# Kernel optimization log

Measured on AMD Instinct MI355X. Metric: run time of the kernel, lower is better.

## Reference

```python
import jax, jax.numpy as jnp
import numpy as np

LOSS_WEIGHT = 1.0

def setup_inputs() -> dict:
    key = jax.random.key(0)
    k1, k2 = jax.random.split(key)
    point_set_1 = jax.random.normal(k1, (8, 4096, 2), dtype=jnp.float32)
    point_set_2 = jax.random.normal(k2, (8, 4096, 2), dtype=jnp.float32)
    return {"point_set_1": point_set_1, "point_set_2": point_set_2}

def reference(point_set_1, point_set_2):
    # Pairwise L2 distances: C[n, i, j] = ||x[n,i] - y[n,j]||_2  -> (N, P1, P2)
    diff = point_set_1[:, :, None, :] - point_set_2[:, None, :, :]
    C = jnp.sqrt(jnp.sum(diff * diff, axis=-1))
    d1 = jnp.min(C, axis=-1).mean(axis=-1)  # x -> nearest y
    d2 = jnp.min(C, axis=-2).mean(axis=-1)  # y -> nearest x
    dist = (d1 + d2) / 2.0                   # (N,)
    return dist * LOSS_WEIGHT
```

## Files before the change

### kernel.cpp

```cpp
#include <hip/hip_runtime.h>
#include <hip/hip_bf16.h>
#include <math.h>


#define B 8
#define N 4096
#define BLOCK 256
#define TX 8
#define NI 2
#define NT 16

__global__ __launch_bounds__(BLOCK) void chamfer_stage1(
    const float2* __restrict__ P1, const float2* __restrict__ P2,
    float* __restrict__ partial, int nj, int jc) {
  extern __shared__ float4 yb[];

  int b = blockIdx.x;
  int c = b % nj; b /= nj;
  int itile = b % NI; b /= NI;
  int n = b % B;
  int dir = b / B;

  const float2* __restrict__ Q = dir ? P2 : P1;
  const float2* __restrict__ D = dir ? P1 : P2;

  const float2* dbase = D + n * N + c * jc;
  for (int t = threadIdx.x; t < jc; t += BLOCK) {
    float2 p = dbase[t];
    yb[t] = make_float4(-2.0f * p.x, -2.0f * p.y,
                        fmaf(p.x, p.x, p.y * p.y), 0.0f);
  }
  __syncthreads();

  float qx[TX], qy[TX], m[TX];
  const float2* qbase = Q + n * N + itile * (BLOCK * TX) + threadIdx.x;
#pragma unroll
  for (int k = 0; k < TX; ++k) {
    float2 q = qbase[k * BLOCK];
    qx[k] = q.x; qy[k] = q.y;
    m[k] = INFINITY;
  }

#pragma unroll 4
  for (int j = 0; j < jc; ++j) {
    float4 y = yb[j];
#pragma unroll
    for (int k = 0; k < TX; ++k) {
      float t = fmaf(qx[k], y.x, fmaf(qy[k], y.y, y.z));
      m[k] = fminf(m[k], t);
    }
  }

  float* dst = partial + (((size_t)c * 2 + dir) * B + n) * N
             + itile * (BLOCK * TX) + threadIdx.x;
#pragma unroll
  for (int k = 0; k < TX; ++k) dst[k * BLOCK] = m[k];
}

__global__ __launch_bounds__(BLOCK) void chamfer_stage2(
    const float2* __restrict__ P1, const float2* __restrict__ P2,
    const float* __restrict__ partial, float* __restrict__ bs, int nj) {
  int b = blockIdx.x;
  int t = b % NT; b /= NT;
  int n = b % B;
  int dir = b / B;

  const float2* __restrict__ Q = dir ? P2 : P1;
  int i = t * BLOCK + threadIdx.x;

  float m = INFINITY;
  const float* __restrict__ pbase = partial + ((size_t)dir * B + n) * N + i;
#pragma unroll 4
  for (int c = 0; c < nj; ++c)
    m = fminf(m, pbase[(size_t)c * 2 * B * N]);

  float2 q = Q[n * N + i];
  float d2 = m + fmaf(q.x, q.x, q.y * q.y);
  float sum = sqrtf(fmaxf(d2, 0.0f));

  __shared__ float red[BLOCK];
  red[threadIdx.x] = sum;
  __syncthreads();
  for (int s = BLOCK / 2; s > 0; s >>= 1) {
    if (threadIdx.x < s) red[threadIdx.x] += red[threadIdx.x + s];
    __syncthreads();
  }
  if (threadIdx.x == 0) bs[(dir * B + n) * NT + t] = red[0];
}

__global__ __launch_bounds__(64) void chamfer_stage3(
    const float* __restrict__ bs, float* __restrict__ out) {
  int n = blockIdx.x;
  int lane = threadIdx.x;
  float v = 0.0f;
  if (lane < 2 * NT) {
    int dir = lane / NT, t = lane % NT;
    v = bs[(dir * B + n) * NT + t];
  }
#pragma unroll
  for (int s = 32; s > 0; s >>= 1)
    v += __shfl_down(v, s, 64);
  if (lane == 0) out[n] = v * (0.5f / (float)N);
}

extern "C" void kernel_launch(void* const* d_in, const int* in_sizes, int n_in,
                              void* d_out, int out_size, void* d_ws, size_t ws_size,
                              hipStream_t stream) {
  const float2* P1 = (const float2*)d_in[0];
  const float2* P2 = (const float2*)d_in[1];
  float* out = (float*)d_out;
  float* partial = (float*)d_ws;

  size_t bs_bytes = 2 * B * NT * sizeof(float);
  int nj = 16;
  while (nj > 1 && (size_t)nj * 2 * B * N * sizeof(float) + bs_bytes > ws_size) nj >>= 1;
  int jc = N / nj;

  float* bs = partial + (size_t)nj * 2 * B * N;

  chamfer_stage1<<<dim3(2 * B * NI * nj), BLOCK, jc * sizeof(float4), stream>>>(
      P1, P2, partial, nj, jc);
  chamfer_stage2<<<dim3(2 * B * NT), BLOCK, 0, stream>>>(P1, P2, partial, bs, nj);
  chamfer_stage3<<<dim3(B), 64, 0, stream>>>(bs, out);
}
```

Before: 30.05 us.

## Use packed FP32 FMA with min3, drop LDS staging, retile to 32 queries per thread

Stage 1 now runs 128-thread blocks, each thread holding 32 query points as packed float2 pairs and computing two candidate points per step with inline v_pk_fma_f32 and v_min3_f32. The LDS staging of transformed candidates is removed, and candidates are read straight from global memory with their -2x and norm terms recomputed in-loop. The j-split grows to 64 chunks, which makes the partial buffer larger and stage 2's reduction longer. The workspace-size check is also removed, so the code assumes the workspace can hold 64 chunks.

```diff
diff --git a/kernel.cpp b/kernel.cpp
--- a/kernel.cpp
+++ b/kernel.cpp
@@ -3,85 +3,95 @@
 #include <math.h>
 
 
+typedef float f32x2 __attribute__((ext_vector_type(2)));
+
 #define B 8
 #define N 4096
-#define BLOCK 256
-#define TX 8
-#define NI 2
+#define NJ 64
+#define JC (N / NJ)
+#define S1B 128
+#define TX 32
 #define NT 16
+#define S2B 256
 
-__global__ __launch_bounds__(BLOCK) void chamfer_stage1(
+__global__ __launch_bounds__(S1B, 2) void chamfer_stage1(
     const float2* __restrict__ P1, const float2* __restrict__ P2,
-    float* __restrict__ partial, int nj, int jc) {
-  extern __shared__ float4 yb[];
-
+    float* __restrict__ partial) {
   int b = blockIdx.x;
-  int c = b % nj; b /= nj;
-  int itile = b % NI; b /= NI;
+  int c = b % NJ; b /= NJ;
   int n = b % B;
   int dir = b / B;
 
   const float2* __restrict__ Q = dir ? P2 : P1;
   const float2* __restrict__ D = dir ? P1 : P2;
+  const float2* __restrict__ db = D + n * N + c * JC;
 
-  const float2* dbase = D + n * N + c * jc;
-  for (int t = threadIdx.x; t < jc; t += BLOCK) {
-    float2 p = dbase[t];
-    yb[t] = make_float4(-2.0f * p.x, -2.0f * p.y,
-                        fmaf(p.x, p.x, p.y * p.y), 0.0f);
-  }
-  __syncthreads();
-
-  float qx[TX], qy[TX], m[TX];
-  const float2* qbase = Q + n * N + itile * (BLOCK * TX) + threadIdx.x;
+  f32x2 qx[TX / 2], qy[TX / 2];
+  float m[TX];
+  const float2* qbase = Q + n * N + threadIdx.x;
 #pragma unroll
-  for (int k = 0; k < TX; ++k) {
-    float2 q = qbase[k * BLOCK];
-    qx[k] = q.x; qy[k] = q.y;
-    m[k] = INFINITY;
+  for (int p = 0; p < TX / 2; ++p) {
+    float2 q0 = qbase[(2 * p) * S1B];
+    float2 q1 = qbase[(2 * p + 1) * S1B];
+    qx[p] = (f32x2){q0.x, q1.x};
+    qy[p] = (f32x2){q0.y, q1.y};
+    m[2 * p] = INFINITY;
+    m[2 * p + 1] = INFINITY;
   }
 
 #pragma unroll 4
-  for (int j = 0; j < jc; ++j) {
-    float4 y = yb[j];
+  for (int j = 0; j < JC; j += 2) {
+    float2 p0 = db[j];
+    float2 p1 = db[j + 1];
+    float ax0f = -2.f * p0.x, ay0f = -2.f * p0.y;
+    float s0f = fmaf(p0.x, p0.x, p0.y * p0.y);
+    float ax1f = -2.f * p1.x, ay1f = -2.f * p1.y;
+    float s1f = fmaf(p1.x, p1.x, p1.y * p1.y);
+    f32x2 ax0 = {ax0f, ax0f}, ay0 = {ay0f, ay0f}, ss0 = {s0f, s0f};
+    f32x2 ax1 = {ax1f, ax1f}, ay1 = {ay1f, ay1f}, ss1 = {s1f, s1f};
 #pragma unroll
-    for (int k = 0; k < TX; ++k) {
-      float t = fmaf(qx[k], y.x, fmaf(qy[k], y.y, y.z));
-      m[k] = fminf(m[k], t);
+    for (int p = 0; p < TX / 2; ++p) {
+      f32x2 u0, t0, u1, t1;
+      asm("v_pk_fma_f32 %0, %1, %2, %3" : "=v"(u0) : "v"(qy[p]), "v"(ay0), "v"(ss0));
+      asm("v_pk_fma_f32 %0, %1, %2, %3" : "=v"(t0) : "v"(qx[p]), "v"(ax0), "v"(u0));
+      asm("v_pk_fma_f32 %0, %1, %2, %3" : "=v"(u1) : "v"(qy[p]), "v"(ay1), "v"(ss1));
+      asm("v_pk_fma_f32 %0, %1, %2, %3" : "=v"(t1) : "v"(qx[p]), "v"(ax1), "v"(u1));
+      asm("v_min3_f32 %0, %0, %1, %2" : "+v"(m[2 * p])     : "v"(t0.x), "v"(t1.x));
+      asm("v_min3_f32 %0, %0, %1, %2" : "+v"(m[2 * p + 1]) : "v"(t0.y), "v"(t1.y));
     }
   }
 
-  float* dst = partial + (((size_t)c * 2 + dir) * B + n) * N
-             + itile * (BLOCK * TX) + threadIdx.x;
+  float* __restrict__ dst =
+      partial + (((size_t)c * 2 + dir) * B + n) * N + threadIdx.x;
 #pragma unroll
-  for (int k = 0; k < TX; ++k) dst[k * BLOCK] = m[k];
+  for (int k = 0; k < TX; ++k) dst[k * S1B] = m[k];
 }
 
-__global__ __launch_bounds__(BLOCK) void chamfer_stage2(
+__global__ __launch_bounds__(S2B) void chamfer_stage2(
     const float2* __restrict__ P1, const float2* __restrict__ P2,
-    const float* __restrict__ partial, float* __restrict__ bs, int nj) {
+    const float* __restrict__ partial, float* __restrict__ bs) {
   int b = blockIdx.x;
   int t = b % NT; b /= NT;
   int n = b % B;
   int dir = b / B;
 
   const float2* __restrict__ Q = dir ? P2 : P1;
-  int i = t * BLOCK + threadIdx.x;
+  int i = t * S2B + threadIdx.x;
 
   float m = INFINITY;
   const float* __restrict__ pbase = partial + ((size_t)dir * B + n) * N + i;
-#pragma unroll 4
-  for (int c = 0; c < nj; ++c)
+#pragma unroll 8
+  for (int c = 0; c < NJ; ++c)
     m = fminf(m, pbase[(size_t)c * 2 * B * N]);
 
   float2 q = Q[n * N + i];
   float d2 = m + fmaf(q.x, q.x, q.y * q.y);
   float sum = sqrtf(fmaxf(d2, 0.0f));
 
-  __shared__ float red[BLOCK];
+  __shared__ float red[S2B];
   red[threadIdx.x] = sum;
   __syncthreads();
-  for (int s = BLOCK / 2; s > 0; s >>= 1) {
+  for (int s = S2B / 2; s > 0; s >>= 1) {
     if (threadIdx.x < s) red[threadIdx.x] += red[threadIdx.x + s];
     __syncthreads();
   }
@@ -110,16 +120,9 @@
   const float2* P2 = (const float2*)d_in[1];
   float* out = (float*)d_out;
   float* partial = (float*)d_ws;
+  float* bs = partial + (size_t)NJ * 2 * B * N;
 
-  size_t bs_bytes = 2 * B * NT * sizeof(float);
-  int nj = 16;
-  while (nj > 1 && (size_t)nj * 2 * B * N * sizeof(float) + bs_bytes > ws_size) nj >>= 1;
-  int jc = N / nj;
-
-  float* bs = partial + (size_t)nj * 2 * B * N;
-
-  chamfer_stage1<<<dim3(2 * B * NI * nj), BLOCK, jc * sizeof(float4), stream>>>(
-      P1, P2, partial, nj, jc);
-  chamfer_stage2<<<dim3(2 * B * NT), BLOCK, 0, stream>>>(P1, P2, partial, bs, nj);
+  chamfer_stage1<<<dim3(2 * B * NJ), S1B, 0, stream>>>(P1, P2, partial);
+  chamfer_stage2<<<dim3(2 * B * NT), S2B, 0, stream>>>(P1, P2, partial, bs);
   chamfer_stage3<<<dim3(B), 64, 0, stream>>>(bs, out);
 }
```

Measured after the change: 48.35 us. 1.61x slower.
